# Optimization experiments

Measured on AMD Instinct MI355X. Metric: run time of the kernel, lower is better.

## Reference

```python
import jax, jax.numpy as jnp
import numpy as np

DIM = 512
LATENT = 1024
BATCH = 128
SEQ = 256


def setup_inputs() -> dict:
    key = jax.random.key(0)
    ks = jax.random.split(key, 7)
    bound = 1.0 / np.sqrt(DIM + LATENT)
    u = lambda k, shape: jax.random.uniform(k, shape, jnp.float32, -bound, bound)
    return {
        "x": jax.random.normal(ks[0], (BATCH, SEQ, DIM), jnp.float32),
        "Wz": u(ks[1], (LATENT, DIM + LATENT)),
        "bz": u(ks[2], (LATENT,)),
        "Wr": u(ks[3], (LATENT, DIM + LATENT)),
        "br": u(ks[4], (LATENT,)),
        "Wi": u(ks[5], (LATENT, DIM + LATENT)),
        "bi": u(ks[6], (LATENT,)),
    }


def reference(x, Wz, bz, Wr, br, Wi, bi):
    # x: [B, T, D]; custom GRU cell, h0 = zeros. Returns stacked hidden
    # history h_1..h_T as [T, B, latent] (torch code returns a list of these).
    B = x.shape[0]
    L = bz.shape[0]
    xt = jnp.swapaxes(x, 0, 1)  # [T, B, D]

    def step(h, xi):
        xh = jnp.concatenate([xi, h], axis=1)                  # [B, D+L]
        zt = jax.nn.sigmoid(xh @ Wz.T + bz)                    # update gate
        rt = jax.nn.sigmoid(xh @ Wr.T + br)                    # reset gate
        xrh = jnp.concatenate([xi, rt * h], axis=1)
        h_new = (1.0 - zt) * h + zt * jnp.tanh(xrh @ Wi.T + bi)
        return h_new, h_new

    h0 = jnp.zeros((B, L), dtype=x.dtype)
    _, h_hist = jax.lax.scan(step, h0, xt)
    return h_hist  # [T, B, L]
```

## Files before the change

kernel.cpp:

```cpp
#include <hip/hip_runtime.h>

typedef __attribute__((ext_vector_type(8))) short short8;
typedef __attribute__((ext_vector_type(4))) float floatx4;
typedef unsigned long long u64;
typedef unsigned short ushort;

#define DEV __device__ __forceinline__

constexpr int B_ = 128, T_ = 256, D_ = 512, L_ = 1024;

constexpr size_t OFF_PREZ = 0;
constexpr size_t OFF_PRER = OFF_PREZ + (size_t)T_ * B_ * L_ * 2;
constexpr size_t OFF_WH   = OFF_PRER + (size_t)T_ * B_ * L_ * 2;
constexpr size_t OFF_WX   = OFF_WH + (size_t)3 * L_ * 1024 * 2;
constexpr size_t OFF_XB   = OFF_WX + (size_t)3 * L_ * 512 * 2;
constexpr size_t OFF_HB   = OFF_XB + (size_t)B_ * T_ * D_ * 2;
constexpr size_t OFF_RH   = OFF_HB + (size_t)B_ * L_ * 2;
constexpr size_t OFF_Z    = OFF_RH + (size_t)B_ * L_ * 2;
constexpr size_t OFF_CTR  = OFF_Z + (size_t)B_ * L_ * 4;

DEV ushort f2bf(float f) {
  unsigned u = __float_as_uint(f);
  u += 0x7fffu + ((u >> 16) & 1u);
  return (ushort)(u >> 16);
}
DEV ushort f2h(float f) { _Float16 h = (_Float16)f; return __builtin_bit_cast(ushort, h); }
DEV float h2f(ushort u) { _Float16 h = __builtin_bit_cast(_Float16, u); return (float)h; }
DEV float sigmoidf_(float x) { return 1.0f / (1.0f + __expf(-x)); }
DEV float tanhf_(float x) {
  float a = fabsf(x);
  float e = __expf(-2.0f * a);
  float t = (1.0f - e) / (1.0f + e);
  return copysignf(t, x);
}

DEV u64 cload64(const void* p) {
  return __hip_atomic_load((const u64*)p, __ATOMIC_RELAXED, __HIP_MEMORY_SCOPE_AGENT);
}
DEV void cstore64(void* p, u64 v) {
  __hip_atomic_store((u64*)p, v, __ATOMIC_RELAXED, __HIP_MEMORY_SCOPE_AGENT);
}

DEV void gld_lds16(const void* g, void* l) {
  __builtin_amdgcn_global_load_lds(
      (const __attribute__((address_space(1))) unsigned int*)g,
      (__attribute__((address_space(3))) unsigned int*)l, 16, 0, 0);
}

DEV u64 prefetch8(const ushort* p) {
  u64 v; asm volatile("global_load_dwordx2 %0, %1, off" : "=v"(v) : "v"(p)); return v;
}
DEV floatx4 prefetch16f(const float* p) {
  floatx4 v; asm volatile("global_load_dwordx4 %0, %1, off" : "=v"(v) : "v"(p)); return v;
}

DEV void gbar_sig(unsigned* flags, int rg, int slot, unsigned iv) {
  asm volatile("s_waitcnt vmcnt(0)" ::: "memory");
  __syncthreads();
  if (threadIdx.x == 0)
    __hip_atomic_store(flags + (((iv & 1) << 3) + rg) * 32 + slot, iv,
                       __ATOMIC_RELAXED, __HIP_MEMORY_SCOPE_AGENT);
}
DEV void gbar_wait(const unsigned* flags, int rg, unsigned iv) {
  if (threadIdx.x < 64) {
    const unsigned* f = flags + (((iv & 1) << 3) + rg) * 32 + (threadIdx.x & 31);
    while (__ballot(__hip_atomic_load(f, __ATOMIC_RELAXED, __HIP_MEMORY_SCOPE_AGENT) != iv))
      __builtin_amdgcn_s_sleep(1);
  }
  __syncthreads();
}

__global__ __launch_bounds__(256) void k_conv_x(const float* __restrict__ x,
                                                unsigned short* __restrict__ xb) {
  size_t i = ((size_t)blockIdx.x * 256 + threadIdx.x) * 8;
  float4 f0 = *(const float4*)(x + i);
  float4 f1 = *(const float4*)(x + i + 4);
  short8 o;
  o[0] = (short)f2bf(f0.x); o[1] = (short)f2bf(f0.y); o[2] = (short)f2bf(f0.z); o[3] = (short)f2bf(f0.w);
  o[4] = (short)f2bf(f1.x); o[5] = (short)f2bf(f1.y); o[6] = (short)f2bf(f1.z); o[7] = (short)f2bf(f1.w);
  *(short8*)&xb[i] = o;
}

__global__ __launch_bounds__(256) void k_conv_w(const float* __restrict__ Wz,
                                                const float* __restrict__ Wr,
                                                const float* __restrict__ Wi,
                                                unsigned short* __restrict__ wx,
                                                unsigned short* __restrict__ wh) {
  int idx = blockIdx.x * 256 + threadIdx.x;
  int g = idx / 196608;
  int rem = idx - g * 196608;
  int n = rem / 192;
  int c = rem - n * 192;
  int k = c * 8;
  const float* W = (g == 0) ? Wz : ((g == 1) ? Wr : Wi);
  const float* src = W + (size_t)n * 1536 + k;
  short8 o;
#pragma unroll
  for (int u = 0; u < 8; ++u) o[u] = (short)f2bf(src[u]);
  if (k < 512)
    *(short8*)&wx[((size_t)g * 1024 + n) * 512 + k] = o;
  else
    *(short8*)&wh[((size_t)g * 1024 + n) * 1024 + (k - 512)] = o;
}

__global__ __launch_bounds__(256) void k_pre_gemm(const unsigned short* __restrict__ xb,
                                                  const unsigned short* __restrict__ wx,
                                                  unsigned short* __restrict__ preZ,
                                                  unsigned short* __restrict__ preR,
                                                  float* __restrict__ outI,
                                                  const float* __restrict__ bz,
                                                  const float* __restrict__ br,
                                                  const float* __restrict__ bi) {
  __shared__ __align__(16) unsigned short As[128 * 64];
  __shared__ __align__(16) unsigned short Bs[128 * 64];
  const int tid = threadIdx.x;
  const int wave = tid >> 6, lane = tid & 63;
  const int m0 = blockIdx.x * 128;
  const int n0g = blockIdx.y * 128;
  const int g = n0g >> 10;
  const int n0 = n0g & 1023;
  const unsigned short* wg = wx + (size_t)g * 1024 * 512;
  const int wm = (wave >> 1) * 64, wn = (wave & 1) * 64;

  floatx4 acc[4][4];
#pragma unroll
  for (int i = 0; i < 4; ++i)
#pragma unroll
    for (int j = 0; j < 4; ++j) acc[i][j] = (floatx4){0.f, 0.f, 0.f, 0.f};

  for (int ko = 0; ko < 8; ++ko) {
    const int k0 = ko * 64;
#pragma unroll
    for (int j = 0; j < 4; ++j) {
      int rowbase = (wave * 4 + j) * 8;
      int row = rowbase + (lane >> 3);
      int clog = (lane & 7) ^ (row & 7);
      gld_lds16(xb + (size_t)(m0 + row) * 512 + k0 + clog * 8, &As[rowbase * 64]);
      gld_lds16(wg + (size_t)(n0 + row) * 512 + k0 + clog * 8, &Bs[rowbase * 64]);
    }
    __syncthreads();
#pragma unroll
    for (int ks = 0; ks < 2; ++ks) {
      short8 a[4], b[4];
      int cl = ks * 4 + (lane >> 4);
#pragma unroll
      for (int i = 0; i < 4; ++i) {
        int r = wm + i * 16 + (lane & 15);
        a[i] = *(const short8*)&As[r * 64 + ((cl ^ (r & 7)) * 8)];
      }
#pragma unroll
      for (int j = 0; j < 4; ++j) {
        int r = wn + j * 16 + (lane & 15);
        b[j] = *(const short8*)&Bs[r * 64 + ((cl ^ (r & 7)) * 8)];
      }
#pragma unroll
      for (int i = 0; i < 4; ++i)
#pragma unroll
        for (int j = 0; j < 4; ++j)
          acc[i][j] = __builtin_amdgcn_mfma_f32_16x16x32_bf16(a[i], b[j], acc[i][j], 0, 0, 0);
    }
    __syncthreads();
  }

  const float* bias = (g == 0) ? bz : ((g == 1) ? br : bi);
#pragma unroll
  for (int i = 0; i < 4; ++i)
#pragma unroll
    for (int j = 0; j < 4; ++j) {
      int ncol = n0 + wn + j * 16 + (lane & 15);
      float bv = bias[ncol];
#pragma unroll
      for (int reg = 0; reg < 4; ++reg) {
        int m = m0 + wm + i * 16 + (lane >> 4) * 4 + reg;
        int bidx = m >> 8, t = m & 255;
        size_t idx = ((size_t)(t * B_ + bidx) << 10) + ncol;
        float v = acc[i][j][reg] + bv;
        if (g == 0)      preZ[idx] = f2h(v);
        else if (g == 1) preR[idx] = f2h(v);
        else             outI[idx] = v;
      }
    }
}

__global__ __launch_bounds__(256, 1) void k_gru(const unsigned short* __restrict__ wh,
                                                const unsigned short* __restrict__ preZ,
                                                const unsigned short* __restrict__ preR,
                                                unsigned short* __restrict__ hb,
                                                unsigned short* __restrict__ rh,
                                                float* __restrict__ out,
                                                unsigned* __restrict__ flags) {
  __shared__ __align__(16) unsigned short WA[64 * 1024];
  __shared__ __align__(16) unsigned short Hs[16 * 512];
  __shared__ __align__(16) float red[512];
  __shared__ __align__(16) float hstash[512];

  const int tid = threadIdx.x, wave = tid >> 6, lane = tid & 63;
  const int p = blockIdx.x;
  const int rg = p >> 5;
  const int slot = p & 31;
  const int r0 = rg * 16;
  const int c0 = slot * 32;

  const unsigned short* wzp = wh + (size_t)c0 * 1024;
  const unsigned short* wrp = wh + (size_t)1048576 + (size_t)c0 * 1024;
  const unsigned short* wip = wh + (size_t)2097152 + (size_t)c0 * 1024;

  for (int idx = tid; idx < 64 * 128; idx += 256) {
    int row = idx >> 7, cl = idx & 127;
    const unsigned short* src = (row < 32) ? (wzp + (size_t)row * 1024 + cl * 8)
                                           : (wrp + (size_t)(row - 32) * 1024 + cl * 8);
    *(short8*)&WA[row * 1024 + ((cl ^ (row & 7))) * 8] = *(const short8*)src;
  }
  hstash[tid] = 0.f;
  hstash[tid + 256] = 0.f;
  __syncthreads();

  const int mrow = lane & 15;
  const int nloc = ((wave & 1) << 4) + ((lane >> 4) << 2);
  const int arow = wave * 16 + mrow;
  const int ax = arow & 7, hx = mrow & 7;
  const unsigned short* preX = (wave < 2) ? preZ : preR;
  const size_t prebase = ((size_t)(r0 + mrow) << 10) + (size_t)(c0 + nloc);
  const unsigned short* hbs = hb + (size_t)r0 * 1024;
  const unsigned short* rhs = rh + (size_t)r0 * 1024;
  const int srow = tid >> 4, scol = tid & 15, sx2 = srow & 7;

  u64 preX8 = *(const u64*)(preX + prebase);
  unsigned bseq = 0;
  float zreg[4] = {0.f, 0.f, 0.f, 0.f};
  float hprev[4] = {0.f, 0.f, 0.f, 0.f};

  for (int t = 0; t < T_; ++t) {
    u64 v[16];
    {
      const unsigned short* src = hbs + (size_t)srow * 1024;
#pragma unroll
      for (int j = 0; j < 8; ++j) v[j]     = cload64(src + (size_t)(scol + j * 16) * 4);
#pragma unroll
      for (int j = 0; j < 8; ++j) v[8 + j] = cload64(src + 512 + (size_t)(scol + j * 16) * 4);
    }
#pragma unroll
    for (int j = 0; j < 8; ++j) {
      int u = scol + j * 16;
      *(u64*)&Hs[srow * 512 + (((u >> 1) ^ sx2)) * 8 + (u & 1) * 4] = v[j];
    }
    __syncthreads();

    floatx4 acc0 = (floatx4){0.f, 0.f, 0.f, 0.f};
    floatx4 acc1 = (floatx4){0.f, 0.f, 0.f, 0.f};
#pragma unroll
    for (int ks = 0; ks < 16; ks += 2) {
      const int ck0 = ks * 4 + (lane >> 4), ck1 = ck0 + 4;
      short8 w0 = *(const short8*)&WA[arow * 1024 + ((ck0 ^ ax)) * 8];
      short8 h0 = *(const short8*)&Hs[mrow * 512 + ((ck0 ^ hx)) * 8];
      acc0 = __builtin_amdgcn_mfma_f32_16x16x32_bf16(w0, h0, acc0, 0, 0, 0);
      short8 w1 = *(const short8*)&WA[arow * 1024 + ((ck1 ^ ax)) * 8];
      short8 h1 = *(const short8*)&Hs[mrow * 512 + ((ck1 ^ hx)) * 8];
      acc1 = __builtin_amdgcn_mfma_f32_16x16x32_bf16(w1, h1, acc1, 0, 0, 0);
    }
    __syncthreads();
#pragma unroll
    for (int j = 0; j < 8; ++j) {
      int u = scol + j * 16;
      *(u64*)&Hs[srow * 512 + (((u >> 1) ^ sx2)) * 8 + (u & 1) * 4] = v[8 + j];
    }
    __syncthreads();
#pragma unroll
    for (int ks = 0; ks < 16; ks += 2) {
      const int ck0 = ks * 4 + (lane >> 4), ck1 = ck0 + 4;
      short8 w0 = *(const short8*)&WA[arow * 1024 + (((64 + ck0) ^ ax)) * 8];
      short8 h0 = *(const short8*)&Hs[mrow * 512 + ((ck0 ^ hx)) * 8];
      acc0 = __builtin_amdgcn_mfma_f32_16x16x32_bf16(w0, h0, acc0, 0, 0, 0);
      short8 w1 = *(const short8*)&WA[arow * 1024 + (((64 + ck1) ^ ax)) * 8];
      short8 h1 = *(const short8*)&Hs[mrow * 512 + ((ck1 ^ hx)) * 8];
      acc1 = __builtin_amdgcn_mfma_f32_16x16x32_bf16(w1, h1, acc1, 0, 0, 0);
    }

    {
      floatx4 accA = acc0 + acc1;
      if (wave < 2) {
#pragma unroll
        for (int r2 = 0; r2 < 4; ++r2)
          zreg[r2] = sigmoidf_(accA[r2] + h2f((ushort)(preX8 >> (16 * r2))));
      } else {
        const floatx4 hp = *(const floatx4*)&hstash[mrow * 32 + nloc];
        u64 o = 0;
#pragma unroll
        for (int r2 = 0; r2 < 4; ++r2) {
          float rg2 = sigmoidf_(accA[r2] + h2f((ushort)(preX8 >> (16 * r2))));
          o |= (u64)f2bf(rg2 * hp[r2]) << (16 * r2);
        }
        cstore64(rh + (size_t)(r0 + mrow) * 1024 + c0 + nloc, o);
      }
    }
    ++bseq;
    gbar_sig(flags, rg, slot, bseq);
    floatx4 preI4 = prefetch16f(out + ((size_t)t << 17) + prebase);
    gbar_wait(flags, rg, bseq);

    {
      const unsigned short* src = rhs + (size_t)srow * 1024;
#pragma unroll
      for (int j = 0; j < 8; ++j) v[j]     = cload64(src + (size_t)(scol + j * 16) * 4);
#pragma unroll
      for (int j = 0; j < 8; ++j) v[8 + j] = cload64(src + 512 + (size_t)(scol + j * 16) * 4);
    }
#pragma unroll
    for (int j = 0; j < 8; ++j) {
      int u = scol + j * 16;
      *(u64*)&Hs[srow * 512 + (((u >> 1) ^ sx2)) * 8 + (u & 1) * 4] = v[j];
    }
    __syncthreads();

    floatx4 accB0 = (floatx4){0.f, 0.f, 0.f, 0.f};
    floatx4 accB1 = (floatx4){0.f, 0.f, 0.f, 0.f};
    const unsigned short* wb = wip + (size_t)(((wave & 1) << 4) + mrow) * 1024 + ((size_t)(wave >> 1) << 9);
    if ((wave >> 1) == 0) {
#pragma unroll
      for (int ks = 0; ks < 16; ks += 2) {
        const int ck0 = ks * 4 + (lane >> 4), ck1 = ck0 + 4;
        short8 w0 = *(const short8*)(wb + ck0 * 8);
        short8 b0 = *(const short8*)&Hs[mrow * 512 + ((ck0 ^ hx)) * 8];
        accB0 = __builtin_amdgcn_mfma_f32_16x16x32_bf16(w0, b0, accB0, 0, 0, 0);
        short8 w1 = *(const short8*)(wb + ck1 * 8);
        short8 b1 = *(const short8*)&Hs[mrow * 512 + ((ck1 ^ hx)) * 8];
        accB1 = __builtin_amdgcn_mfma_f32_16x16x32_bf16(w1, b1, accB1, 0, 0, 0);
      }
    }
    __syncthreads();
#pragma unroll
    for (int j = 0; j < 8; ++j) {
      int u = scol + j * 16;
      *(u64*)&Hs[srow * 512 + (((u >> 1) ^ sx2)) * 8 + (u & 1) * 4] = v[8 + j];
    }
    __syncthreads();
    if ((wave >> 1) == 1) {
#pragma unroll
      for (int ks = 0; ks < 16; ks += 2) {
        const int ck0 = ks * 4 + (lane >> 4), ck1 = ck0 + 4;
        short8 w0 = *(const short8*)(wb + ck0 * 8);
        short8 b0 = *(const short8*)&Hs[mrow * 512 + ((ck0 ^ hx)) * 8];
        accB0 = __builtin_amdgcn_mfma_f32_16x16x32_bf16(w0, b0, accB0, 0, 0, 0);
        short8 w1 = *(const short8*)(wb + ck1 * 8);
        short8 b1 = *(const short8*)&Hs[mrow * 512 + ((ck1 ^ hx)) * 8];
        accB1 = __builtin_amdgcn_mfma_f32_16x16x32_bf16(w1, b1, accB1, 0, 0, 0);
      }
      floatx4 sB = accB0 + accB1;
      *(floatx4*)&red[((wave - 2) << 8) + (lane << 2)] = sB;
    }
    __syncthreads();
    if (wave < 2) {
      floatx4 accB = accB0 + accB1 + *(const floatx4*)&red[(wave << 8) + (lane << 2)];
      float hn[4];
      u64 ob = 0;
#pragma unroll
      for (int r2 = 0; r2 < 4; ++r2) {
        float ivl = tanhf_(accB[r2] + preI4[r2]);
        hn[r2] = (1.f - zreg[r2]) * hprev[r2] + zreg[r2] * ivl;
        hprev[r2] = hn[r2];
        ob |= (u64)f2bf(hn[r2]) << (16 * r2);
      }
      float* po = out + ((size_t)t << 17) + prebase;
      *(floatx4*)po = (floatx4){hn[0], hn[1], hn[2], hn[3]};
      cstore64(hb + (size_t)(r0 + mrow) * 1024 + c0 + nloc, ob);
      *(floatx4*)&hstash[mrow * 32 + nloc] = (floatx4){hn[0], hn[1], hn[2], hn[3]};
    }

    if (t + 1 < T_) {
      ++bseq;
      gbar_sig(flags, rg, slot, bseq);
      preX8 = prefetch8(preX + ((size_t)(t + 1) << 17) + prebase);
      gbar_wait(flags, rg, bseq);
    }
  }
}

extern "C" void kernel_launch(void* const* d_in, const int* in_sizes, int n_in,
                              void* d_out, int out_size, void* d_ws, size_t ws_size,
                              hipStream_t stream) {
  const float* x  = (const float*)d_in[0];
  const float* Wz = (const float*)d_in[1];
  const float* bz = (const float*)d_in[2];
  const float* Wr = (const float*)d_in[3];
  const float* br = (const float*)d_in[4];
  const float* Wi = (const float*)d_in[5];
  const float* bi = (const float*)d_in[6];
  float* out = (float*)d_out;
  char* wsb = (char*)d_ws;

  unsigned short* preZ = (unsigned short*)(wsb + OFF_PREZ);
  unsigned short* preR = (unsigned short*)(wsb + OFF_PRER);
  unsigned short* wh   = (unsigned short*)(wsb + OFF_WH);
  unsigned short* wx   = (unsigned short*)(wsb + OFF_WX);
  unsigned short* xb   = (unsigned short*)(wsb + OFF_XB);
  unsigned short* hb   = (unsigned short*)(wsb + OFF_HB);
  unsigned short* rh   = (unsigned short*)(wsb + OFF_RH);
  unsigned* flags      = (unsigned*)(wsb + OFF_CTR);

  hipMemsetAsync(wsb + OFF_HB, 0, (size_t)B_ * L_ * 2, stream);
  hipMemsetAsync(wsb + OFF_CTR, 0, 16384, stream);

  k_conv_x<<<8192, 256, 0, stream>>>(x, xb);
  k_conv_w<<<2304, 256, 0, stream>>>(Wz, Wr, Wi, wx, wh);
  k_pre_gemm<<<dim3(256, 24), 256, 0, stream>>>(xb, wx, preZ, preR, out, bz, br, bi);
  k_gru<<<256, 256, 0, stream>>>(wh, preZ, preR, hb, rh, out, flags);
}
```

Before: 2.487 ms.

## Hold recurrent weights in registers and stage full hidden row in LDS

Moves the per-block recurrent weight slices for the z/r gates and the candidate gate out of LDS and global memory into per-lane register fragments loaded once before the time loop. The LDS hidden-state buffer is doubled so the whole 1024-wide row is staged in one pass, which removes the half-split restaging and its extra barriers. The cross-wave reduction buffer for the candidate matmul goes away, and waves 0-1 now do that full K loop on their own. The aim is fewer barriers and fewer LDS/global weight reads per step. The cost is very high VGPR use (64 short8 fragments per lane) and more serial MFMA work on two waves.

```diff
diff --git a/kernel.cpp b/kernel.cpp
--- a/kernel.cpp
+++ b/kernel.cpp
@@ -3,6 +3,7 @@
 typedef __attribute__((ext_vector_type(8))) short short8;
 typedef __attribute__((ext_vector_type(4))) float floatx4;
 typedef unsigned long long u64;
+typedef __attribute__((ext_vector_type(2))) unsigned long long u64x2;
 typedef unsigned short ushort;
 
 #define DEV __device__ __forceinline__
@@ -189,92 +190,83 @@
                                                 unsigned short* __restrict__ rh,
                                                 float* __restrict__ out,
                                                 unsigned* __restrict__ flags) {
-  __shared__ __align__(16) unsigned short WA[64 * 1024];
-  __shared__ __align__(16) unsigned short Hs[16 * 512];
-  __shared__ __align__(16) float red[512];
+  __shared__ __align__(16) unsigned short Hs[16 * 1024];
   __shared__ __align__(16) float hstash[512];
 
   const int tid = threadIdx.x, wave = tid >> 6, lane = tid & 63;
   const int p = blockIdx.x;
-  const int rg = p >> 5;
-  const int slot = p & 31;
-  const int r0 = rg * 16;
-  const int c0 = slot * 32;
-
-  const unsigned short* wzp = wh + (size_t)c0 * 1024;
-  const unsigned short* wrp = wh + (size_t)1048576 + (size_t)c0 * 1024;
-  const unsigned short* wip = wh + (size_t)2097152 + (size_t)c0 * 1024;
-
-  for (int idx = tid; idx < 64 * 128; idx += 256) {
-    int row = idx >> 7, cl = idx & 127;
-    const unsigned short* src = (row < 32) ? (wzp + (size_t)row * 1024 + cl * 8)
-                                           : (wrp + (size_t)(row - 32) * 1024 + cl * 8);
-    *(short8*)&WA[row * 1024 + ((cl ^ (row & 7))) * 8] = *(const short8*)src;
-  }
+  const int rg = p >> 5, slot = p & 31;
+  const int r0 = rg * 16, c0 = slot * 32;
+
+  const int mrow = lane & 15;
+  const int cksub = lane >> 4;
+  const int hx = mrow & 7;
+  const int nloc = ((wave & 1) << 4) + (cksub << 2);
+
+  const unsigned short* wAp = wh + ((wave < 2) ? (size_t)0 : (size_t)1048576)
+                                 + (size_t)(c0 + ((wave & 1) << 4) + mrow) * 1024;
+  const unsigned short* wBp = wh + (size_t)2097152
+                                 + (size_t)(c0 + ((wave & 1) << 4) + mrow) * 1024;
+  short8 wfA[32], wfB[32];
+#pragma unroll
+  for (int h = 0; h < 2; ++h)
+#pragma unroll
+    for (int s = 0; s < 8; ++s) {
+      const int cb = h * 64 + s * 8 + cksub;
+      wfA[h * 16 + s * 2]     = *(const short8*)&wAp[cb * 8];
+      wfA[h * 16 + s * 2 + 1] = *(const short8*)&wAp[(cb + 4) * 8];
+      wfB[h * 16 + s * 2]     = *(const short8*)&wBp[cb * 8];
+      wfB[h * 16 + s * 2 + 1] = *(const short8*)&wBp[(cb + 4) * 8];
+    }
+
   hstash[tid] = 0.f;
   hstash[tid + 256] = 0.f;
   __syncthreads();
 
-  const int mrow = lane & 15;
-  const int nloc = ((wave & 1) << 4) + ((lane >> 4) << 2);
-  const int arow = wave * 16 + mrow;
-  const int ax = arow & 7, hx = mrow & 7;
   const unsigned short* preX = (wave < 2) ? preZ : preR;
   const size_t prebase = ((size_t)(r0 + mrow) << 10) + (size_t)(c0 + nloc);
   const unsigned short* hbs = hb + (size_t)r0 * 1024;
   const unsigned short* rhs = rh + (size_t)r0 * 1024;
   const int srow = tid >> 4, scol = tid & 15, sx2 = srow & 7;
 
+  auto stage = [&](const unsigned short* base) {
+    const unsigned short* src = base + (size_t)srow * 1024;
+    u64 v[16];
+#pragma unroll
+    for (int j = 0; j < 8; ++j) {
+      const int c = scol + j * 16;
+      v[2 * j]     = cload64(src + c * 8);
+      v[2 * j + 1] = cload64(src + c * 8 + 4);
+    }
+#pragma unroll
+    for (int j = 0; j < 8; ++j) {
+      const int c = scol + j * 16;
+      u64x2 tq; tq.x = v[2 * j]; tq.y = v[2 * j + 1];
+      *(short8*)&Hs[srow * 1024 + ((c ^ sx2) * 8)] = __builtin_bit_cast(short8, tq);
+    }
+  };
+
   u64 preX8 = *(const u64*)(preX + prebase);
   unsigned bseq = 0;
   float zreg[4] = {0.f, 0.f, 0.f, 0.f};
   float hprev[4] = {0.f, 0.f, 0.f, 0.f};
 
   for (int t = 0; t < T_; ++t) {
-    u64 v[16];
-    {
-      const unsigned short* src = hbs + (size_t)srow * 1024;
-#pragma unroll
-      for (int j = 0; j < 8; ++j) v[j]     = cload64(src + (size_t)(scol + j * 16) * 4);
-#pragma unroll
-      for (int j = 0; j < 8; ++j) v[8 + j] = cload64(src + 512 + (size_t)(scol + j * 16) * 4);
-    }
-#pragma unroll
-    for (int j = 0; j < 8; ++j) {
-      int u = scol + j * 16;
-      *(u64*)&Hs[srow * 512 + (((u >> 1) ^ sx2)) * 8 + (u & 1) * 4] = v[j];
-    }
+    stage(hbs);
     __syncthreads();
 
     floatx4 acc0 = (floatx4){0.f, 0.f, 0.f, 0.f};
     floatx4 acc1 = (floatx4){0.f, 0.f, 0.f, 0.f};
 #pragma unroll
-    for (int ks = 0; ks < 16; ks += 2) {
-      const int ck0 = ks * 4 + (lane >> 4), ck1 = ck0 + 4;
-      short8 w0 = *(const short8*)&WA[arow * 1024 + ((ck0 ^ ax)) * 8];
-      short8 h0 = *(const short8*)&Hs[mrow * 512 + ((ck0 ^ hx)) * 8];
-      acc0 = __builtin_amdgcn_mfma_f32_16x16x32_bf16(w0, h0, acc0, 0, 0, 0);
-      short8 w1 = *(const short8*)&WA[arow * 1024 + ((ck1 ^ ax)) * 8];
-      short8 h1 = *(const short8*)&Hs[mrow * 512 + ((ck1 ^ hx)) * 8];
-      acc1 = __builtin_amdgcn_mfma_f32_16x16x32_bf16(w1, h1, acc1, 0, 0, 0);
-    }
-    __syncthreads();
-#pragma unroll
-    for (int j = 0; j < 8; ++j) {
-      int u = scol + j * 16;
-      *(u64*)&Hs[srow * 512 + (((u >> 1) ^ sx2)) * 8 + (u & 1) * 4] = v[8 + j];
-    }
-    __syncthreads();
-#pragma unroll
-    for (int ks = 0; ks < 16; ks += 2) {
-      const int ck0 = ks * 4 + (lane >> 4), ck1 = ck0 + 4;
-      short8 w0 = *(const short8*)&WA[arow * 1024 + (((64 + ck0) ^ ax)) * 8];
-      short8 h0 = *(const short8*)&Hs[mrow * 512 + ((ck0 ^ hx)) * 8];
-      acc0 = __builtin_amdgcn_mfma_f32_16x16x32_bf16(w0, h0, acc0, 0, 0, 0);
-      short8 w1 = *(const short8*)&WA[arow * 1024 + (((64 + ck1) ^ ax)) * 8];
-      short8 h1 = *(const short8*)&Hs[mrow * 512 + ((ck1 ^ hx)) * 8];
-      acc1 = __builtin_amdgcn_mfma_f32_16x16x32_bf16(w1, h1, acc1, 0, 0, 0);
-    }
+    for (int h = 0; h < 2; ++h)
+#pragma unroll
+      for (int s = 0; s < 8; ++s) {
+        const int ck0 = h * 64 + s * 8 + cksub;
+        short8 h0 = *(const short8*)&Hs[mrow * 1024 + ((ck0 ^ hx) * 8)];
+        acc0 = __builtin_amdgcn_mfma_f32_16x16x32_bf16(wfA[h * 16 + s * 2], h0, acc0, 0, 0, 0);
+        short8 h1 = *(const short8*)&Hs[mrow * 1024 + (((ck0 + 4) ^ hx) * 8)];
+        acc1 = __builtin_amdgcn_mfma_f32_16x16x32_bf16(wfA[h * 16 + s * 2 + 1], h1, acc1, 0, 0, 0);
+      }
 
     {
       floatx4 accA = acc0 + acc1;
@@ -298,59 +290,23 @@
     floatx4 preI4 = prefetch16f(out + ((size_t)t << 17) + prebase);
     gbar_wait(flags, rg, bseq);
 
-    {
-      const unsigned short* src = rhs + (size_t)srow * 1024;
-#pragma unroll
-      for (int j = 0; j < 8; ++j) v[j]     = cload64(src + (size_t)(scol + j * 16) * 4);
-#pragma unroll
-      for (int j = 0; j < 8; ++j) v[8 + j] = cload64(src + 512 + (size_t)(scol + j * 16) * 4);
-    }
-#pragma unroll
-    for (int j = 0; j < 8; ++j) {
-      int u = scol + j * 16;
-      *(u64*)&Hs[srow * 512 + (((u >> 1) ^ sx2)) * 8 + (u & 1) * 4] = v[j];
-    }
+    stage(rhs);
     __syncthreads();
 
-    floatx4 accB0 = (floatx4){0.f, 0.f, 0.f, 0.f};
-    floatx4 accB1 = (floatx4){0.f, 0.f, 0.f, 0.f};
-    const unsigned short* wb = wip + (size_t)(((wave & 1) << 4) + mrow) * 1024 + ((size_t)(wave >> 1) << 9);
-    if ((wave >> 1) == 0) {
-#pragma unroll
-      for (int ks = 0; ks < 16; ks += 2) {
-        const int ck0 = ks * 4 + (lane >> 4), ck1 = ck0 + 4;
-        short8 w0 = *(const short8*)(wb + ck0 * 8);
-        short8 b0 = *(const short8*)&Hs[mrow * 512 + ((ck0 ^ hx)) * 8];
-        accB0 = __builtin_amdgcn_mfma_f32_16x16x32_bf16(w0, b0, accB0, 0, 0, 0);
-        short8 w1 = *(const short8*)(wb + ck1 * 8);
-        short8 b1 = *(const short8*)&Hs[mrow * 512 + ((ck1 ^ hx)) * 8];
-        accB1 = __builtin_amdgcn_mfma_f32_16x16x32_bf16(w1, b1, accB1, 0, 0, 0);
-      }
-    }
-    __syncthreads();
-#pragma unroll
-    for (int j = 0; j < 8; ++j) {
-      int u = scol + j * 16;
-      *(u64*)&Hs[srow * 512 + (((u >> 1) ^ sx2)) * 8 + (u & 1) * 4] = v[8 + j];
-    }
-    __syncthreads();
-    if ((wave >> 1) == 1) {
-#pragma unroll
-      for (int ks = 0; ks < 16; ks += 2) {
-        const int ck0 = ks * 4 + (lane >> 4), ck1 = ck0 + 4;
-        short8 w0 = *(const short8*)(wb + ck0 * 8);
-        short8 b0 = *(const short8*)&Hs[mrow * 512 + ((ck0 ^ hx)) * 8];
-        accB0 = __builtin_amdgcn_mfma_f32_16x16x32_bf16(w0, b0, accB0, 0, 0, 0);
-        short8 w1 = *(const short8*)(wb + ck1 * 8);
-        short8 b1 = *(const short8*)&Hs[mrow * 512 + ((ck1 ^ hx)) * 8];
-        accB1 = __builtin_amdgcn_mfma_f32_16x16x32_bf16(w1, b1, accB1, 0, 0, 0);
-      }
-      floatx4 sB = accB0 + accB1;
-      *(floatx4*)&red[((wave - 2) << 8) + (lane << 2)] = sB;
-    }
-    __syncthreads();
     if (wave < 2) {
-      floatx4 accB = accB0 + accB1 + *(const floatx4*)&red[(wave << 8) + (lane << 2)];
+      floatx4 accB0 = (floatx4){0.f, 0.f, 0.f, 0.f};
+      floatx4 accB1 = (floatx4){0.f, 0.f, 0.f, 0.f};
+#pragma unroll
+      for (int h = 0; h < 2; ++h)
+#pragma unroll
+        for (int s = 0; s < 8; ++s) {
+          const int ck0 = h * 64 + s * 8 + cksub;
+          short8 b0 = *(const short8*)&Hs[mrow * 1024 + ((ck0 ^ hx) * 8)];
+          accB0 = __builtin_amdgcn_mfma_f32_16x16x32_bf16(wfB[h * 16 + s * 2], b0, accB0, 0, 0, 0);
+          short8 b1 = *(const short8*)&Hs[mrow * 1024 + (((ck0 + 4) ^ hx) * 8)];
+          accB1 = __builtin_amdgcn_mfma_f32_16x16x32_bf16(wfB[h * 16 + s * 2 + 1], b1, accB1, 0, 0, 0);
+        }
+      floatx4 accB = accB0 + accB1;
       float hn[4];
       u64 ob = 0;
 #pragma unroll
```

Measured after the change: 2.196 ms. 11.7% less time.
